# Optimization experiments

Measured on AMD Instinct MI355X. Metric: run time of the kernel, lower is better.

The kernel has to match this reference:

```python
import jax, jax.numpy as jnp
import numpy as np

HIDDEN = 1024
EMB = 256
VOCAB = 500000
B = 4096
C = 128
EPS = 1e-12


def setup_inputs() -> dict:
    key = jax.random.key(0)
    ks = jax.random.split(key, 8)
    hidden_states = jax.random.normal(ks[0], (B, HIDDEN), dtype=jnp.float32)
    cand_idx = jax.random.randint(ks[1], (B, C), 0, VOCAB, dtype=jnp.int32)
    W_dense = jax.random.normal(ks[2], (EMB, HIDDEN), dtype=jnp.float32) * (1.0 / np.sqrt(HIDDEN))
    b_dense = jnp.zeros((EMB,), dtype=jnp.float32)
    ln_gamma = jnp.ones((EMB,), dtype=jnp.float32)
    ln_beta = jnp.zeros((EMB,), dtype=jnp.float32)
    decoder_table = jax.random.normal(ks[3], (VOCAB, EMB), dtype=jnp.float32) * 0.02
    entity_bias = jnp.zeros((VOCAB,), dtype=jnp.float32)
    return {
        "hidden_states": hidden_states,
        "W_dense": W_dense,
        "b_dense": b_dense,
        "ln_gamma": ln_gamma,
        "ln_beta": ln_beta,
        "decoder_table": decoder_table,
        "entity_bias": entity_bias,
        "cand_idx": cand_idx,
    }


def _transform(x, W_dense, b_dense, ln_gamma, ln_beta):
    # Linear hidden_size -> entity_emb_size, gelu, LayerNorm
    h = x @ W_dense.T + b_dense
    h = jax.nn.gelu(h, approximate=False)
    mu = jnp.mean(h, axis=-1, keepdims=True)
    var = jnp.mean(jnp.square(h - mu), axis=-1, keepdims=True)
    return (h - mu) * jax.lax.rsqrt(var + EPS) * ln_gamma + ln_beta


def reference(hidden_states, W_dense, b_dense, ln_gamma, ln_beta, decoder_table, entity_bias, cand_idx):
    h = _transform(hidden_states, W_dense, b_dense, ln_gamma, ln_beta)  # [B, EMB]
    cand_emb = decoder_table[cand_idx]          # [B, C, EMB] ragged gather (padded)
    bias = entity_bias[cand_idx]                # [B, C]
    scores = jnp.einsum('bce,be->bc', cand_emb, h) + bias  # [B, C]
    return scores
```

## Files before the change

kernel.cpp:

```cpp
#include <hip/hip_runtime.h>
#include <hip/hip_bf16.h>
#include <math.h>

#define HIDDEN 1024
#define EMB    256
#define BROWS  4096
#define CAND   128
#define LN_EPS 1e-12f

typedef __attribute__((ext_vector_type(8))) short bf16x8;
typedef __attribute__((ext_vector_type(4))) float f32x4;

__device__ __forceinline__ int swz(int row, int slot) { return slot ^ ((row >> 1) & 3); }

__device__ __forceinline__ unsigned short f2bf(float f) {
    __bf16 h = (__bf16)f;
    return __builtin_bit_cast(unsigned short, h);
}

__global__ __launch_bounds__(256) void k_transform(
    const float* __restrict__ A,
    const float* __restrict__ W,
    const float* __restrict__ bias,
    const float* __restrict__ gamma,
    const float* __restrict__ beta,
    float* __restrict__ G)
{
    __shared__ unsigned short As[16 * 32];
    __shared__ unsigned short Ws[256 * 32];
    __shared__ float part[16][8];

    const int tid  = threadIdx.x;
    const int lane = tid & 63;
    const int wv   = tid >> 6;
    const int m0   = blockIdx.x * 16;

    const int lcol = lane & 15;
    const int lk   = lane >> 4;

    f32x4 acc[4] = {};

    for (int kt = 0; kt < HIDDEN; kt += 32) {
        float4 a0, a1;
        const int arow = tid >> 2, apr = tid & 3;
        if (tid < 64) {
            a0 = *(const float4*)&A[(size_t)(m0 + arow) * HIDDEN + kt + apr * 8];
            a1 = *(const float4*)&A[(size_t)(m0 + arow) * HIDDEN + kt + apr * 8 + 4];
        }
        float4 w0[4], w1[4];
        #pragma unroll
        for (int i = 0; i < 4; ++i) {
            int id = tid + i * 256;
            int row = id >> 2, pr = id & 3;
            w0[i] = *(const float4*)&W[(size_t)row * HIDDEN + kt + pr * 8];
            w1[i] = *(const float4*)&W[(size_t)row * HIDDEN + kt + pr * 8 + 4];
        }
        __syncthreads();
        if (tid < 64) {
            bf16x8 v;
            v[0]=f2bf(a0.x); v[1]=f2bf(a0.y); v[2]=f2bf(a0.z); v[3]=f2bf(a0.w);
            v[4]=f2bf(a1.x); v[5]=f2bf(a1.y); v[6]=f2bf(a1.z); v[7]=f2bf(a1.w);
            *(bf16x8*)&As[arow * 32 + swz(arow, apr) * 8] = v;
        }
        #pragma unroll
        for (int i = 0; i < 4; ++i) {
            int id = tid + i * 256;
            int row = id >> 2, pr = id & 3;
            bf16x8 v;
            v[0]=f2bf(w0[i].x); v[1]=f2bf(w0[i].y); v[2]=f2bf(w0[i].z); v[3]=f2bf(w0[i].w);
            v[4]=f2bf(w1[i].x); v[5]=f2bf(w1[i].y); v[6]=f2bf(w1[i].z); v[7]=f2bf(w1[i].w);
            *(bf16x8*)&Ws[row * 32 + swz(row, pr) * 8] = v;
        }
        __syncthreads();
        bf16x8 af = *(const bf16x8*)&As[lcol * 32 + swz(lcol, lk) * 8];
        bf16x8 bfr[4];
        #pragma unroll
        for (int n = 0; n < 4; ++n) {
            int r = wv * 64 + n * 16 + lcol;
            bfr[n] = *(const bf16x8*)&Ws[r * 32 + swz(r, lk) * 8];
        }
        #pragma unroll
        for (int n = 0; n < 4; ++n)
            acc[n] = __builtin_amdgcn_mfma_f32_16x16x32_bf16(af, bfr[n], acc[n], 0, 0, 0);
    }

    float bcol[4], gcol[4], becol[4];
    #pragma unroll
    for (int n = 0; n < 4; ++n) {
        int col = wv * 64 + n * 16 + lcol;
        bcol[n]  = bias[col];
        gcol[n]  = gamma[col];
        becol[n] = beta[col];
    }

    float sv[4] = {}, qv[4] = {};
    #pragma unroll
    for (int n = 0; n < 4; ++n) {
        #pragma unroll
        for (int r = 0; r < 4; ++r) {
            float v = acc[n][r] + bcol[n];
            v = 0.5f * v * (1.0f + erff(v * 0.70710678118654752f));
            acc[n][r] = v;
            sv[r] += v;
            qv[r] += v * v;
        }
    }
    #pragma unroll
    for (int r = 0; r < 4; ++r) {
        #pragma unroll
        for (int msk = 8; msk >= 1; msk >>= 1) {
            sv[r] += __shfl_xor(sv[r], msk);
            qv[r] += __shfl_xor(qv[r], msk);
        }
    }
    if (lcol == 0) {
        #pragma unroll
        for (int r = 0; r < 4; ++r) {
            int R = lk * 4 + r;
            part[R][wv * 2 + 0] = sv[r];
            part[R][wv * 2 + 1] = qv[r];
        }
    }
    __syncthreads();

    #pragma unroll
    for (int r = 0; r < 4; ++r) {
        int R = lk * 4 + r;
        float4 p0 = *(const float4*)&part[R][0];
        float4 p1 = *(const float4*)&part[R][4];
        float s  = p0.x + p0.z + p1.x + p1.z;
        float q  = p0.y + p0.w + p1.y + p1.w;
        float mu = s * (1.0f / 256.0f);
        float var = q * (1.0f / 256.0f) - mu * mu;
        float rs = rsqrtf(var + LN_EPS);
        #pragma unroll
        for (int n = 0; n < 4; ++n) {
            int col = wv * 64 + n * 16 + lcol;
            G[(size_t)(m0 + R) * EMB + col] = (acc[n][r] - mu) * rs * gcol[n] + becol[n];
        }
    }
}

__global__ __launch_bounds__(256) void k_scores(
    const float* __restrict__ H,
    const float* __restrict__ table,
    const float* __restrict__ ebias,
    const int*   __restrict__ cidx,
    float* __restrict__ out)
{
    __shared__ float smem[16384];
    const int tid  = threadIdx.x;
    const int lane = tid & 63;
    const int wv   = tid >> 6;
    const int l    = lane & 15;
    const int q    = lane >> 4;
    const int b     = blockIdx.x >> 1;
    const int cbase = (blockIdx.x & 1) * 64 + wv * 16;

    const float4* Hrow = (const float4*)(H + (size_t)b * EMB);
    float4 hv[4];
    #pragma unroll
    for (int p = 0; p < 4; ++p) hv[p] = Hrow[p * 16 + l];

    const int sidxv = cidx[(size_t)b * CAND + cbase + l];
    const float ebv = ebias[sidxv];

    float* wbase = &smem[wv * 4096];
    #pragma unroll
    for (int r = 0; r < 16; ++r) {
        int idx = __shfl(sidxv, r);
        const float* gsrc = table + (size_t)idx * EMB + lane * 4;
        __builtin_amdgcn_global_load_lds(
            (const __attribute__((address_space(1))) void*)gsrc,
            (__attribute__((address_space(3))) void*)(wbase + r * 256),
            16, 0, 0);
    }

    float res[4];
#define DOGROUP(g, WN)                                                        \
    {                                                                         \
        asm volatile("s_waitcnt vmcnt(" WN ")" ::: "memory");                 \
        const float4* row = (const float4*)(wbase + (4 * (g) + q) * 256);     \
        float s = 0.f;                                                        \
        _Pragma("unroll")                                                     \
        for (int p = 0; p < 4; ++p) {                                         \
            float4 t = row[p * 16 + l];                                       \
            s += t.x * hv[p].x + t.y * hv[p].y + t.z * hv[p].z + t.w * hv[p].w;\
        }                                                                     \
        _Pragma("unroll")                                                     \
        for (int m = 8; m >= 1; m >>= 1) s += __shfl_xor(s, m);               \
        res[g] = s;                                                           \
    }
    DOGROUP(0, "12")
    DOGROUP(1, "8")
    DOGROUP(2, "4")
    DOGROUP(3, "0")
#undef DOGROUP

    #pragma unroll
    for (int g = 0; g < 4; ++g) {
        float eb = __shfl(ebv, 4 * g + q);
        if (l == 0) out[(size_t)b * CAND + cbase + 4 * g + q] = res[g] + eb;
    }
}

extern "C" void kernel_launch(void* const* d_in, const int* in_sizes, int n_in,
                              void* d_out, int out_size, void* d_ws, size_t ws_size,
                              hipStream_t stream) {
    const float* hidden = (const float*)d_in[0];
    const float* Wd     = (const float*)d_in[1];
    const float* bd     = (const float*)d_in[2];
    const float* gamma  = (const float*)d_in[3];
    const float* beta   = (const float*)d_in[4];
    const float* table  = (const float*)d_in[5];
    const float* ebias  = (const float*)d_in[6];
    const int*   cidx   = (const int*)d_in[7];
    float* out = (float*)d_out;

    float* G = (float*)d_ws;

    k_transform<<<dim3(BROWS / 16), 256, 0, stream>>>(hidden, Wd, bd, gamma, beta, G);
    k_scores<<<dim3(BROWS * 2), 256, 0, stream>>>(G, table, ebias, cidx, out);
}
```

Measured before the change: 135.2 us.

## Split transform GEMM along K into partial sums with separate LayerNorm finalize

The dense projection is split four ways along the hidden dimension. This quadruples the block count from 256 so the GPU's many CUs are better occupied. Each split writes fp32 partial sums to workspace, and a new finalize kernel sums them, applies bias, GELU and LayerNorm with a two-pass variance. The GEMM loop also prefetches the next K tile into registers while MFMAs run on the current tile. In exchange it adds an extra kernel launch and about 16 MB of partial-sum traffic.

```diff
diff --git a/kernel.cpp b/kernel.cpp
--- a/kernel.cpp
+++ b/kernel.cpp
@@ -18,43 +18,48 @@
     return __builtin_bit_cast(unsigned short, h);
 }
 
-__global__ __launch_bounds__(256) void k_transform(
+__device__ __forceinline__ float gelu(float x) {
+    return 0.5f * x * (1.0f + erff(x * 0.70710678118654752f));
+}
+
+__global__ __launch_bounds__(256) void k_gemm_partial(
     const float* __restrict__ A,
     const float* __restrict__ W,
-    const float* __restrict__ bias,
-    const float* __restrict__ gamma,
-    const float* __restrict__ beta,
-    float* __restrict__ G)
+    float* __restrict__ P)
 {
     __shared__ unsigned short As[16 * 32];
     __shared__ unsigned short Ws[256 * 32];
-    __shared__ float part[16][8];
 
     const int tid  = threadIdx.x;
     const int lane = tid & 63;
     const int wv   = tid >> 6;
     const int m0   = blockIdx.x * 16;
+    const int ks   = blockIdx.y;
+    const int kbeg = ks * 256;
 
     const int lcol = lane & 15;
     const int lk   = lane >> 4;
+    const int arow = tid >> 2, apr = tid & 3;
+
+    float4 a0, a1, w0[4], w1[4];
+
+#define LOADREGS(KT)                                                          \
+    if (tid < 64) {                                                           \
+        a0 = *(const float4*)&A[(size_t)(m0 + arow) * HIDDEN + (KT) + apr * 8];     \
+        a1 = *(const float4*)&A[(size_t)(m0 + arow) * HIDDEN + (KT) + apr * 8 + 4]; \
+    }                                                                         \
+    _Pragma("unroll")                                                         \
+    for (int i = 0; i < 4; ++i) {                                             \
+        int id = tid + i * 256;                                               \
+        int row = id >> 2, pr = id & 3;                                       \
+        w0[i] = *(const float4*)&W[(size_t)row * HIDDEN + (KT) + pr * 8];     \
+        w1[i] = *(const float4*)&W[(size_t)row * HIDDEN + (KT) + pr * 8 + 4]; \
+    }
 
     f32x4 acc[4] = {};
-
-    for (int kt = 0; kt < HIDDEN; kt += 32) {
-        float4 a0, a1;
-        const int arow = tid >> 2, apr = tid & 3;
-        if (tid < 64) {
-            a0 = *(const float4*)&A[(size_t)(m0 + arow) * HIDDEN + kt + apr * 8];
-            a1 = *(const float4*)&A[(size_t)(m0 + arow) * HIDDEN + kt + apr * 8 + 4];
-        }
-        float4 w0[4], w1[4];
-        #pragma unroll
-        for (int i = 0; i < 4; ++i) {
-            int id = tid + i * 256;
-            int row = id >> 2, pr = id & 3;
-            w0[i] = *(const float4*)&W[(size_t)row * HIDDEN + kt + pr * 8];
-            w1[i] = *(const float4*)&W[(size_t)row * HIDDEN + kt + pr * 8 + 4];
-        }
+    LOADREGS(kbeg)
+
+    for (int it = 0; it < 8; ++it) {
         __syncthreads();
         if (tid < 64) {
             bf16x8 v;
@@ -72,6 +77,7 @@
             *(bf16x8*)&Ws[row * 32 + swz(row, pr) * 8] = v;
         }
         __syncthreads();
+        if (it < 7) { LOADREGS(kbeg + (it + 1) * 32) }
         bf16x8 af = *(const bf16x8*)&As[lcol * 32 + swz(lcol, lk) * 8];
         bf16x8 bfr[4];
         #pragma unroll
@@ -83,62 +89,63 @@
         for (int n = 0; n < 4; ++n)
             acc[n] = __builtin_amdgcn_mfma_f32_16x16x32_bf16(af, bfr[n], acc[n], 0, 0, 0);
     }
-
-    float bcol[4], gcol[4], becol[4];
-    #pragma unroll
-    for (int n = 0; n < 4; ++n) {
-        int col = wv * 64 + n * 16 + lcol;
-        bcol[n]  = bias[col];
-        gcol[n]  = gamma[col];
-        becol[n] = beta[col];
-    }
-
-    float sv[4] = {}, qv[4] = {};
-    #pragma unroll
-    for (int n = 0; n < 4; ++n) {
+#undef LOADREGS
+
+    float* Pout = P + (size_t)ks * ((size_t)BROWS * EMB);
+    #pragma unroll
+    for (int n = 0; n < 4; ++n)
         #pragma unroll
         for (int r = 0; r < 4; ++r) {
-            float v = acc[n][r] + bcol[n];
-            v = 0.5f * v * (1.0f + erff(v * 0.70710678118654752f));
-            acc[n][r] = v;
-            sv[r] += v;
-            qv[r] += v * v;
-        }
-    }
-    #pragma unroll
-    for (int r = 0; r < 4; ++r) {
-        #pragma unroll
-        for (int msk = 8; msk >= 1; msk >>= 1) {
-            sv[r] += __shfl_xor(sv[r], msk);
-            qv[r] += __shfl_xor(qv[r], msk);
-        }
-    }
-    if (lcol == 0) {
-        #pragma unroll
-        for (int r = 0; r < 4; ++r) {
-            int R = lk * 4 + r;
-            part[R][wv * 2 + 0] = sv[r];
-            part[R][wv * 2 + 1] = qv[r];
-        }
-    }
-    __syncthreads();
-
-    #pragma unroll
-    for (int r = 0; r < 4; ++r) {
-        int R = lk * 4 + r;
-        float4 p0 = *(const float4*)&part[R][0];
-        float4 p1 = *(const float4*)&part[R][4];
-        float s  = p0.x + p0.z + p1.x + p1.z;
-        float q  = p0.y + p0.w + p1.y + p1.w;
-        float mu = s * (1.0f / 256.0f);
-        float var = q * (1.0f / 256.0f) - mu * mu;
-        float rs = rsqrtf(var + LN_EPS);
-        #pragma unroll
-        for (int n = 0; n < 4; ++n) {
+            int R   = lk * 4 + r;
             int col = wv * 64 + n * 16 + lcol;
-            G[(size_t)(m0 + R) * EMB + col] = (acc[n][r] - mu) * rs * gcol[n] + becol[n];
-        }
-    }
+            Pout[(size_t)(m0 + R) * EMB + col] = acc[n][r];
+        }
+}
+
+__global__ __launch_bounds__(256) void k_finalize(
+    const float* __restrict__ P,
+    const float* __restrict__ bias,
+    const float* __restrict__ gamma,
+    const float* __restrict__ beta,
+    float* __restrict__ G)
+{
+    const int tid  = threadIdx.x;
+    const int lane = tid & 63;
+    const int row  = blockIdx.x * 4 + (tid >> 6);
+    const size_t off = (size_t)row * EMB + lane * 4;
+    const size_t S   = (size_t)BROWS * EMB;
+
+    float4 v0 = *(const float4*)&P[off];
+    float4 v1 = *(const float4*)&P[off + S];
+    float4 v2 = *(const float4*)&P[off + 2 * S];
+    float4 v3 = *(const float4*)&P[off + 3 * S];
+    float4 bb = *(const float4*)&bias[lane * 4];
+
+    float4 h;
+    h.x = gelu(v0.x + v1.x + v2.x + v3.x + bb.x);
+    h.y = gelu(v0.y + v1.y + v2.y + v3.y + bb.y);
+    h.z = gelu(v0.z + v1.z + v2.z + v3.z + bb.z);
+    h.w = gelu(v0.w + v1.w + v2.w + v3.w + bb.w);
+
+    float s = h.x + h.y + h.z + h.w;
+    #pragma unroll
+    for (int m = 32; m >= 1; m >>= 1) s += __shfl_xor(s, m);
+    const float mu = s * (1.0f / 256.0f);
+
+    const float dx = h.x - mu, dy = h.y - mu, dz = h.z - mu, dw = h.w - mu;
+    float q = dx * dx + dy * dy + dz * dz + dw * dw;
+    #pragma unroll
+    for (int m = 32; m >= 1; m >>= 1) q += __shfl_xor(q, m);
+    const float rs = rsqrtf(q * (1.0f / 256.0f) + LN_EPS);
+
+    float4 g  = *(const float4*)&gamma[lane * 4];
+    float4 be = *(const float4*)&beta[lane * 4];
+    float4 o;
+    o.x = dx * rs * g.x + be.x;
+    o.y = dy * rs * g.y + be.y;
+    o.z = dz * rs * g.z + be.z;
+    o.w = dw * rs * g.w + be.w;
+    *(float4*)&G[off] = o;
 }
 
 __global__ __launch_bounds__(256) void k_scores(
@@ -217,8 +224,11 @@
     const int*   cidx   = (const int*)d_in[7];
     float* out = (float*)d_out;
 
-    float* G = (float*)d_ws;
-
-    k_transform<<<dim3(BROWS / 16), 256, 0, stream>>>(hidden, Wd, bd, gamma, beta, G);
+    char* ws = (char*)d_ws;
+    float* G = (float*)ws;
+    float* P = (float*)(ws + 4 * 1024 * 1024);
+
+    k_gemm_partial<<<dim3(BROWS / 16, 4), 256, 0, stream>>>(hidden, Wd, P);
+    k_finalize<<<dim3(BROWS / 4), 256, 0, stream>>>(P, bd, gamma, beta, G);
     k_scores<<<dim3(BROWS * 2), 256, 0, stream>>>(G, table, ebias, cidx, out);
 }
```

After: 119.7 us (median of 2 runs). -11.5%, faster.
